# Performance work log

Hardware: AMD Instinct MI355X
Metric: run time of the kernel (lower is better)

## Reference

```python
import jax, jax.numpy as jnp
import numpy as np

# DCNv4 config (matches init_kwargs)
C = 64; G = 4; GC = C // G          # group channels = 16
KS = 3; KP = KS * KS                # 9 sampling points per group
DIL = 1; OFFSET_SCALE = 1.0
OM_DIM = int(np.ceil(G * KP * 3 / 8) * 8)  # 112 (padded offset+mask dim)
N, H, W = 4, 128, 128


def setup_inputs() -> dict:
    key = jax.random.key(0)
    ks = jax.random.split(key, 5)
    x = jax.random.normal(ks[0], (N, C, H, W), dtype=jnp.float32)
    value_w = jax.random.normal(ks[1], (C, C), dtype=jnp.float32) * (1.0 / np.sqrt(C))
    value_b = jnp.zeros((C,), dtype=jnp.float32)
    # small random offset/mask projection (torch zero-init would be degenerate)
    om_w = jax.random.normal(ks[2], (OM_DIM, C), dtype=jnp.float32) * 0.02
    om_b = jax.random.normal(ks[3], (OM_DIM,), dtype=jnp.float32) * 0.02
    out_w = jax.random.normal(ks[4], (C, C), dtype=jnp.float32) * (1.0 / np.sqrt(C))
    out_b = jnp.zeros((C,), dtype=jnp.float32)
    return {"x": x, "value_w": value_w, "value_b": value_b,
            "om_w": om_w, "om_b": om_b, "out_w": out_w, "out_b": out_b}


def _dcnv4_core(v, off, mask, Hh, Ww):
    # v: (N, L, G, GC)   off: (N, L, G, KP, 2) (x,y)   mask: (N, L, G, KP)
    n, L = v.shape[0], v.shape[1]
    py = (jnp.arange(L) // Ww).astype(jnp.float32)          # (L,)
    px = (jnp.arange(L) % Ww).astype(jnp.float32)
    r = (KS - 1) // 2
    dy, dx = jnp.meshgrid(jnp.arange(-r, r + 1, dtype=jnp.float32) * DIL,
                          jnp.arange(-r, r + 1, dtype=jnp.float32) * DIL,
                          indexing="ij")
    dy = dy.reshape(-1); dx = dx.reshape(-1)                # (KP,)
    # sampling coords: (N, L, G, KP)
    sy = py[None, :, None, None] + dy[None, None, None, :] + off[..., 1] * OFFSET_SCALE
    sx = px[None, :, None, None] + dx[None, None, None, :] + off[..., 0] * OFFSET_SCALE

    y0 = jnp.floor(sy); x0 = jnp.floor(sx)
    wy = sy - y0; wx = sx - x0
    vg = v.transpose(0, 2, 1, 3)                            # (N, G, L, GC)

    def gather(yc, xc, wgt):
        valid = ((yc >= 0) & (yc < Hh) & (xc >= 0) & (xc < Ww)).astype(v.dtype)
        yi = jnp.clip(yc, 0, Hh - 1).astype(jnp.int32)
        xi = jnp.clip(xc, 0, Ww - 1).astype(jnp.int32)
        idx = (yi * Ww + xi).transpose(0, 2, 1, 3).reshape(n, G, L * KP)  # (N,G,L*KP)
        g = jnp.take_along_axis(vg, idx[..., None], axis=2)              # (N,G,L*KP,GC)
        w = (wgt * valid).transpose(0, 2, 1, 3).reshape(n, G, L * KP, 1)
        return g * w

    samp = (gather(y0, x0, (1 - wy) * (1 - wx))
            + gather(y0, x0 + 1, (1 - wy) * wx)
            + gather(y0 + 1, x0, wy * (1 - wx))
            + gather(y0 + 1, x0 + 1, wy * wx))               # (N,G,L*KP,GC)
    samp = samp.reshape(n, G, L, KP, GC)
    m = mask.transpose(0, 2, 1, 3)[..., None]                # (N,G,L,KP,1)
    out = (samp * m).sum(axis=3)                             # (N,G,L,GC)
    return out.transpose(0, 2, 1, 3).reshape(n, L, G * GC)


def reference(x, value_w, value_b, om_w, om_b, out_w, out_b):
    n, c, Hh, Ww = x.shape
    L = Hh * Ww
    inp = x.transpose(0, 2, 3, 1).reshape(n, L, c)           # (N, L, C)
    v = (inp @ value_w.T + value_b).reshape(n, L, G, GC)     # value_proj
    om = inp @ om_w.T + om_b                                 # (N, L, 112)
    om = om[..., :G * KP * 3].reshape(n, L, G, KP * 3)       # per-group [off(2K), mask(K)]
    off = om[..., :2 * KP].reshape(n, L, G, KP, 2)
    mask = om[..., 2 * KP:]                                  # no softmax in DCNv4
    y = _dcnv4_core(v, off, mask, Hh, Ww)                    # (N, L, C)
    y = y @ out_w.T + out_b                                  # output_proj
    return y.reshape(n, Hh, Ww, c).transpose(0, 3, 1, 2)     # (N, C, H, W)
```

## Files before the change

### kernel.cpp

```cpp
#include <hip/hip_runtime.h>

#define NN 4
#define CC 64
#define GG 4
#define GCC 16
#define HH 128
#define WW 128
#define LL (HH*WW)
#define OMS 112
#define WPC 192

__global__ void pack_kernel(const float* __restrict__ value_w, const float* __restrict__ value_b,
                            const float* __restrict__ om_w,    const float* __restrict__ om_b,
                            const float* __restrict__ out_w,
                            float* __restrict__ wpack, float* __restrict__ bpack,
                            float* __restrict__ owt)
{
  const int i = blockIdx.x * 256 + threadIdx.x;
  if (i < 64 * WPC) {
    const int k = i / WPC, c = i % WPC;
    float v = 0.0f;
    if (c < 64) v = value_w[c * 64 + k];
    else if (c < 176) {
      const int s = c - 64;
      if (s % 28 != 27) { const int r = s - s / 28; v = om_w[r * 64 + k]; }
    }
    wpack[i] = v;
  }
  if (i < WPC) {
    float v = 0.0f;
    if (i < 64) v = value_b[i];
    else if (i < 176) {
      const int s = i - 64;
      if (s % 28 != 27) { const int r = s - s / 28; v = om_b[r]; }
    }
    bpack[i] = v;
  }
  if (i < 64 * 64) {
    const int k = i >> 6, c = i & 63;
    owt[i] = out_w[c * 64 + k];
  }
}

__global__ __launch_bounds__(256) void vm_kernel(
    const float* __restrict__ x, const float* __restrict__ wpack,
    const float* __restrict__ bpack,
    float* __restrict__ vws, float* __restrict__ omws)
{
  __shared__ float wlds[64][16];
  const int t    = threadIdx.x;
  const int ch   = blockIdx.y;
  const int col0 = ch << 4;

  {
    const int k = t >> 2, q = t & 3;
    *(float4*)&wlds[k][q * 4] =
        *(const float4*)&wpack[k * WPC + col0 + q * 4];
  }
  float b[16];
  #pragma unroll
  for (int j = 0; j < 16; ++j) b[j] = bpack[col0 + j];
  __syncthreads();

  const int l0 = blockIdx.x << 10;
  const int n  = l0 >> 14;
  const int hw = (l0 & (LL - 1)) + t;

  float acc[4][16];
  #pragma unroll
  for (int pi = 0; pi < 4; ++pi)
    #pragma unroll
    for (int j = 0; j < 16; ++j) acc[pi][j] = b[j];

  const float* xb = x + (size_t)n * CC * LL + hw;
  #pragma unroll 8
  for (int k = 0; k < 64; ++k) {
    float xv[4];
    #pragma unroll
    for (int pi = 0; pi < 4; ++pi) xv[pi] = xb[(size_t)k * LL + pi * 256];
    #pragma unroll
    for (int q = 0; q < 4; ++q) {
      const float4 w = *(const float4*)&wlds[k][q * 4];
      #pragma unroll
      for (int pi = 0; pi < 4; ++pi) {
        acc[pi][q*4+0] = fmaf(xv[pi], w.x, acc[pi][q*4+0]);
        acc[pi][q*4+1] = fmaf(xv[pi], w.y, acc[pi][q*4+1]);
        acc[pi][q*4+2] = fmaf(xv[pi], w.z, acc[pi][q*4+2]);
        acc[pi][q*4+3] = fmaf(xv[pi], w.w, acc[pi][q*4+3]);
      }
    }
  }

  float* dst; int col; int stride;
  if (ch < 4) { dst = vws  + (size_t)n * LL * 64;  col = col0;      stride = 64;  }
  else        { dst = omws + (size_t)n * LL * OMS; col = col0 - 64; stride = OMS; }
  #pragma unroll
  for (int pi = 0; pi < 4; ++pi) {
    float* d = dst + (size_t)(hw + pi * 256) * stride + col;
    #pragma unroll
    for (int q = 0; q < 4; ++q)
      *(float4*)&d[q * 4] =
          make_float4(acc[pi][q*4+0], acc[pi][q*4+1], acc[pi][q*4+2], acc[pi][q*4+3]);
  }
}

__global__ __launch_bounds__(512) void dcn_kernel(
    const float* __restrict__ vws, const float* __restrict__ omws,
    const float* __restrict__ owt, const float* __restrict__ out_b,
    float* __restrict__ out)
{
  __shared__ float s_lds[32][68];
  __shared__ float owlds[64 * 64];
  const int t   = threadIdx.x;
  const int B   = blockIdx.x;
  const int xcd = B & 7;
  const int n   = xcd >> 1;
  const int idx = ((xcd & 1) << 8) | (B >> 3);
  const int row = idx >> 2;
  const int l0  = (row << 7) + ((idx & 3) << 5);

  {
    const float4* s4 = (const float4*)owt;
    float4*       d4 = (float4*)owlds;
    d4[t]       = s4[t];
    d4[512 + t] = s4[512 + t];
  }

  {
    const int px = t >> 4;
    const int g  = (t >> 2) & 3;
    const int qq = t & 3;
    const int l  = l0 + px;
    const float pyf = (float)row;
    const float pxf = (float)(l & (WW - 1));
    const float* __restrict__ omp_  = omws + ((size_t)n * LL + l) * OMS + g * 28;
    const float* __restrict__ vbase = vws + (size_t)n * LL * CC + g * GCC + qq * 4;

    float buf[28];
    const float4* og4 = (const float4*)omp_;
    #pragma unroll
    for (int i = 0; i < 7; ++i) {
      const float4 vv = og4[i];
      buf[4*i+0] = vv.x; buf[4*i+1] = vv.y; buf[4*i+2] = vv.z; buf[4*i+3] = vv.w;
    }

    float s0 = 0.0f, s1 = 0.0f, s2 = 0.0f, s3 = 0.0f;

    #pragma unroll
    for (int pp = 0; pp < 9; ++pp) {
      const float sy  = pyf + (float)(pp / 3 - 1) + buf[2*pp+1];
      const float sx  = pxf + (float)(pp % 3 - 1) + buf[2*pp+0];
      const float y0f = floorf(sy), x0f = floorf(sx);
      const float wy  = sy - y0f,  wx  = sx - x0f;
      const int   iy  = (int)y0f,  ix  = (int)x0f;
      const float m   = buf[18 + pp];
      const float w00 = (1.0f - wy) * (1.0f - wx) * m;
      const float w01 = (1.0f - wy) * wx * m;
      const float w10 = wy * (1.0f - wx) * m;
      const float w11 = wy * wx * m;
      #pragma unroll
      for (int cor = 0; cor < 4; ++cor) {
        const int   cy = iy + (cor >> 1);
        const int   cx = ix + (cor & 1);
        const float w  = (cor == 0) ? w00 : (cor == 1) ? w01 : (cor == 2) ? w10 : w11;
        if (cy >= 0 && cy < HH && cx >= 0 && cx < WW) {
          const float4 vv = *(const float4*)(vbase + (size_t)(cy * WW + cx) * CC);
          s0 = fmaf(w, vv.x, s0);
          s1 = fmaf(w, vv.y, s1);
          s2 = fmaf(w, vv.z, s2);
          s3 = fmaf(w, vv.w, s3);
        }
      }
    }
    *(float4*)&s_lds[px][g * 16 + qq * 4] = make_float4(s0, s1, s2, s3);
  }
  __syncthreads();

  {
    const int px = t & 31;
    const int c4 = t >> 5;
    const int l  = l0 + px;
    float y0 = out_b[c4 * 4 + 0], y1 = out_b[c4 * 4 + 1];
    float y2 = out_b[c4 * 4 + 2], y3 = out_b[c4 * 4 + 3];
    #pragma unroll 4
    for (int k4 = 0; k4 < 16; ++k4) {
      const float4 sv = *(const float4*)&s_lds[px][k4 * 4];
      #pragma unroll
      for (int e = 0; e < 4; ++e) {
        const float se = (e == 0) ? sv.x : (e == 1) ? sv.y : (e == 2) ? sv.z : sv.w;
        const float4 wv = *(const float4*)&owlds[(k4 * 4 + e) * 64 + c4 * 4];
        y0 = fmaf(se, wv.x, y0);
        y1 = fmaf(se, wv.y, y1);
        y2 = fmaf(se, wv.z, y2);
        y3 = fmaf(se, wv.w, y3);
      }
    }
    float* op = out + ((size_t)n * CC) * LL + l;
    op[(size_t)(c4 * 4 + 0) * LL] = y0;
    op[(size_t)(c4 * 4 + 1) * LL] = y1;
    op[(size_t)(c4 * 4 + 2) * LL] = y2;
    op[(size_t)(c4 * 4 + 3) * LL] = y3;
  }
}

extern "C" void kernel_launch(void* const* d_in, const int* in_sizes, int n_in,
                              void* d_out, int out_size, void* d_ws, size_t ws_size,
                              hipStream_t stream) {
  const float* x       = (const float*)d_in[0];
  const float* value_w = (const float*)d_in[1];
  const float* value_b = (const float*)d_in[2];
  const float* om_w    = (const float*)d_in[3];
  const float* om_b    = (const float*)d_in[4];
  const float* out_w   = (const float*)d_in[5];
  const float* out_b   = (const float*)d_in[6];
  float* outp = (float*)d_out;

  float* vws   = (float*)d_ws;
  float* omws  = vws   + (size_t)NN * LL * CC;
  float* wpack = omws  + (size_t)NN * LL * OMS;
  float* bpack = wpack + 64 * WPC;
  float* owt   = bpack + WPC;

  pack_kernel<<<dim3(48), dim3(256), 0, stream>>>(
      value_w, value_b, om_w, om_b, out_w, wpack, bpack, owt);
  vm_kernel<<<dim3(64, 11), dim3(256), 0, stream>>>(
      x, wpack, bpack, vws, omws);
  dcn_kernel<<<dim3(2048), dim3(512), 0, stream>>>(
      vws, omws, owt, out_b, outp);
}
```

Baseline: 151.1 us.

## Use split-bf16 MFMA for input and output projections

```diff
diff --git a/kernel.cpp b/kernel.cpp
--- a/kernel.cpp
+++ b/kernel.cpp
@@ -10,107 +10,138 @@
 #define OMS 112
 #define WPC 192
 
+typedef __attribute__((ext_vector_type(8))) short bf16x8;
+typedef __attribute__((ext_vector_type(4))) float f32x4;
+
+static __device__ __forceinline__ unsigned short f2bf(float x) {
+  union { float f; unsigned u; } v; v.f = x;
+  unsigned r = v.u + 0x7fff + ((v.u >> 16) & 1);
+  return (unsigned short)(r >> 16);
+}
+static __device__ __forceinline__ float bf2f(unsigned short s) {
+  union { float f; unsigned u; } v; v.u = ((unsigned)s) << 16; return v.f;
+}
+static __device__ __forceinline__ void split2(float x, unsigned short& h, unsigned short& l) {
+  h = f2bf(x);
+  l = f2bf(x - bf2f(h));
+}
+
 __global__ void pack_kernel(const float* __restrict__ value_w, const float* __restrict__ value_b,
                             const float* __restrict__ om_w,    const float* __restrict__ om_b,
                             const float* __restrict__ out_w,
-                            float* __restrict__ wpack, float* __restrict__ bpack,
-                            float* __restrict__ owt)
+                            unsigned short* __restrict__ wphi, unsigned short* __restrict__ wplo,
+                            unsigned short* __restrict__ owhi, unsigned short* __restrict__ owlo,
+                            float* __restrict__ bpack)
 {
   const int i = blockIdx.x * 256 + threadIdx.x;
-  if (i < 64 * WPC) {
-    const int k = i / WPC, c = i % WPC;
+  if (i < WPC * 64) {
+    const int c = i >> 6, k = i & 63;
     float v = 0.0f;
     if (c < 64) v = value_w[c * 64 + k];
     else if (c < 176) {
       const int s = c - 64;
-      if (s % 28 != 27) { const int r = s - s / 28; v = om_w[r * 64 + k]; }
-    }
-    wpack[i] = v;
+      if (s % 28 != 27) v = om_w[(s - s / 28) * 64 + k];
+    }
+    unsigned short h, l; split2(v, h, l);
+    wphi[i] = h; wplo[i] = l;
+  }
+  if (i < 64 * 64) {
+    unsigned short h, l; split2(out_w[i], h, l);
+    owhi[i] = h; owlo[i] = l;
   }
   if (i < WPC) {
     float v = 0.0f;
     if (i < 64) v = value_b[i];
-    else if (i < 176) {
-      const int s = i - 64;
-      if (s % 28 != 27) { const int r = s - s / 28; v = om_b[r]; }
-    }
+    else if (i < 176) { const int s = i - 64; if (s % 28 != 27) v = om_b[s - s / 28]; }
     bpack[i] = v;
   }
-  if (i < 64 * 64) {
-    const int k = i >> 6, c = i & 63;
-    owt[i] = out_w[c * 64 + k];
-  }
 }
 
 __global__ __launch_bounds__(256) void vm_kernel(
-    const float* __restrict__ x, const float* __restrict__ wpack,
+    const float* __restrict__ x,
+    const unsigned short* __restrict__ wphi, const unsigned short* __restrict__ wplo,
     const float* __restrict__ bpack,
     float* __restrict__ vws, float* __restrict__ omws)
 {
-  __shared__ float wlds[64][16];
-  const int t    = threadIdx.x;
-  const int ch   = blockIdx.y;
-  const int col0 = ch << 4;
-
-  {
-    const int k = t >> 2, q = t & 3;
-    *(float4*)&wlds[k][q * 4] =
-        *(const float4*)&wpack[k * WPC + col0 + q * 4];
-  }
-  float b[16];
+  __shared__ unsigned short ahi[128][72];
+  __shared__ unsigned short alo[128][72];
+  const int t   = threadIdx.x;
+  const int sid = blockIdx.x;
+  const int n   = sid >> 7;
+  const int ll0 = (sid & 127) << 7;
+  const size_t gl0 = (size_t)sid << 7;
+
+  {
+    const float* xb = x + (size_t)n * CC * LL + ll0;
+    #pragma unroll
+    for (int i = 0; i < 4; ++i) {
+      const int pid = t + i * 256;
+      const int c   = (pid >> 5) << 1;
+      const int px4 = (pid & 31) << 2;
+      const float4 a = *(const float4*)(xb + (size_t)c * LL + px4);
+      const float4 b = *(const float4*)(xb + (size_t)(c + 1) * LL + px4);
+      const float av[4] = {a.x, a.y, a.z, a.w};
+      const float bv[4] = {b.x, b.y, b.z, b.w};
+      #pragma unroll
+      for (int e = 0; e < 4; ++e) {
+        unsigned short ha, la, hb, lb;
+        split2(av[e], ha, la); split2(bv[e], hb, lb);
+        *(unsigned*)&ahi[px4 + e][c] = (unsigned)ha | ((unsigned)hb << 16);
+        *(unsigned*)&alo[px4 + e][c] = (unsigned)la | ((unsigned)lb << 16);
+      }
+    }
+  }
+  __syncthreads();
+
+  const int w  = t >> 6;
+  const int ln = t & 63;
+  const int ct = blockIdx.y * 4 + w;
+  const int c0 = ct << 4;
+  const int r  = ln & 15;
+  const int kq = ln >> 4;
+
+  bf16x8 Bh[2], Bl[2];
   #pragma unroll
-  for (int j = 0; j < 16; ++j) b[j] = bpack[col0 + j];
-  __syncthreads();
-
-  const int l0 = blockIdx.x << 10;
-  const int n  = l0 >> 14;
-  const int hw = (l0 & (LL - 1)) + t;
-
-  float acc[4][16];
+  for (int ks = 0; ks < 2; ++ks) {
+    Bh[ks] = *(const bf16x8*)&wphi[(c0 + r) * 64 + ks * 32 + kq * 8];
+    Bl[ks] = *(const bf16x8*)&wplo[(c0 + r) * 64 + ks * 32 + kq * 8];
+  }
+  const float bias = bpack[c0 + r];
+
   #pragma unroll
-  for (int pi = 0; pi < 4; ++pi)
-    #pragma unroll
-    for (int j = 0; j < 16; ++j) acc[pi][j] = b[j];
-
-  const float* xb = x + (size_t)n * CC * LL + hw;
-  #pragma unroll 8
-  for (int k = 0; k < 64; ++k) {
-    float xv[4];
-    #pragma unroll
-    for (int pi = 0; pi < 4; ++pi) xv[pi] = xb[(size_t)k * LL + pi * 256];
-    #pragma unroll
-    for (int q = 0; q < 4; ++q) {
-      const float4 w = *(const float4*)&wlds[k][q * 4];
-      #pragma unroll
-      for (int pi = 0; pi < 4; ++pi) {
-        acc[pi][q*4+0] = fmaf(xv[pi], w.x, acc[pi][q*4+0]);
-        acc[pi][q*4+1] = fmaf(xv[pi], w.y, acc[pi][q*4+1]);
-        acc[pi][q*4+2] = fmaf(xv[pi], w.z, acc[pi][q*4+2]);
-        acc[pi][q*4+3] = fmaf(xv[pi], w.w, acc[pi][q*4+3]);
-      }
-    }
-  }
-
-  float* dst; int col; int stride;
-  if (ch < 4) { dst = vws  + (size_t)n * LL * 64;  col = col0;      stride = 64;  }
-  else        { dst = omws + (size_t)n * LL * OMS; col = col0 - 64; stride = OMS; }
-  #pragma unroll
-  for (int pi = 0; pi < 4; ++pi) {
-    float* d = dst + (size_t)(hw + pi * 256) * stride + col;
-    #pragma unroll
-    for (int q = 0; q < 4; ++q)
-      *(float4*)&d[q * 4] =
-          make_float4(acc[pi][q*4+0], acc[pi][q*4+1], acc[pi][q*4+2], acc[pi][q*4+3]);
-  }
-}
-
-__global__ __launch_bounds__(512) void dcn_kernel(
+  for (int pt = 0; pt < 8; ++pt) {
+    bf16x8 Ah[2], Al[2];
+    #pragma unroll
+    for (int ks = 0; ks < 2; ++ks) {
+      Ah[ks] = *(const bf16x8*)&ahi[pt * 16 + r][ks * 32 + kq * 8];
+      Al[ks] = *(const bf16x8*)&alo[pt * 16 + r][ks * 32 + kq * 8];
+    }
+    f32x4 acc = {bias, bias, bias, bias};
+    #pragma unroll
+    for (int ks = 0; ks < 2; ++ks) {
+      acc = __builtin_amdgcn_mfma_f32_16x16x32_bf16(Al[ks], Bh[ks], acc, 0, 0, 0);
+      acc = __builtin_amdgcn_mfma_f32_16x16x32_bf16(Ah[ks], Bl[ks], acc, 0, 0, 0);
+      acc = __builtin_amdgcn_mfma_f32_16x16x32_bf16(Ah[ks], Bh[ks], acc, 0, 0, 0);
+    }
+    if (ct < 4) {
+      float* d = vws + (gl0 + pt * 16 + kq * 4) * 64 + c0 + r;
+      d[0] = acc[0]; d[64] = acc[1]; d[128] = acc[2]; d[192] = acc[3];
+    } else if (ct < 11) {
+      float* d = omws + (gl0 + pt * 16 + kq * 4) * (size_t)OMS + (c0 - 64) + r;
+      d[0] = acc[0]; d[OMS] = acc[1]; d[2 * OMS] = acc[2]; d[3 * OMS] = acc[3];
+    }
+  }
+}
+
+__global__ __launch_bounds__(512, 4) void dcn_kernel(
     const float* __restrict__ vws, const float* __restrict__ omws,
-    const float* __restrict__ owt, const float* __restrict__ out_b,
+    const unsigned short* __restrict__ owhi, const unsigned short* __restrict__ owlo,
+    const float* __restrict__ out_b,
     float* __restrict__ out)
 {
-  __shared__ float s_lds[32][68];
-  __shared__ float owlds[64 * 64];
+  __shared__ unsigned short shi[32][72];
+  __shared__ unsigned short slo[32][72];
+  __shared__ float y_lds[32][68];
   const int t   = threadIdx.x;
   const int B   = blockIdx.x;
   const int xcd = B & 7;
@@ -120,16 +151,7 @@
   const int l0  = (row << 7) + ((idx & 3) << 5);
 
   {
-    const float4* s4 = (const float4*)owt;
-    float4*       d4 = (float4*)owlds;
-    d4[t]       = s4[t];
-    d4[512 + t] = s4[512 + t];
-  }
-
-  {
-    const int px = t >> 4;
-    const int g  = (t >> 2) & 3;
-    const int qq = t & 3;
+    const int px = t >> 4, g = (t >> 2) & 3, qq = t & 3;
     const int l  = l0 + px;
     const float pyf = (float)row;
     const float pxf = (float)(l & (WW - 1));
@@ -145,7 +167,6 @@
     }
 
     float s0 = 0.0f, s1 = 0.0f, s2 = 0.0f, s3 = 0.0f;
-
     #pragma unroll
     for (int pp = 0; pp < 9; ++pp) {
       const float sy  = pyf + (float)(pp / 3 - 1) + buf[2*pp+1];
@@ -162,44 +183,54 @@
       for (int cor = 0; cor < 4; ++cor) {
         const int   cy = iy + (cor >> 1);
         const int   cx = ix + (cor & 1);
-        const float w  = (cor == 0) ? w00 : (cor == 1) ? w01 : (cor == 2) ? w10 : w11;
+        const float wgt = (cor == 0) ? w00 : (cor == 1) ? w01 : (cor == 2) ? w10 : w11;
         if (cy >= 0 && cy < HH && cx >= 0 && cx < WW) {
           const float4 vv = *(const float4*)(vbase + (size_t)(cy * WW + cx) * CC);
-          s0 = fmaf(w, vv.x, s0);
-          s1 = fmaf(w, vv.y, s1);
-          s2 = fmaf(w, vv.z, s2);
-          s3 = fmaf(w, vv.w, s3);
+          s0 = fmaf(wgt, vv.x, s0);
+          s1 = fmaf(wgt, vv.y, s1);
+          s2 = fmaf(wgt, vv.z, s2);
+          s3 = fmaf(wgt, vv.w, s3);
         }
       }
     }
-    *(float4*)&s_lds[px][g * 16 + qq * 4] = make_float4(s0, s1, s2, s3);
+    unsigned short h0,u0,h1,u1,h2,u2,h3,u3;
+    split2(s0,h0,u0); split2(s1,h1,u1); split2(s2,h2,u2); split2(s3,h3,u3);
+    *(ushort4*)&shi[px][g * 16 + qq * 4] = make_ushort4(h0, h1, h2, h3);
+    *(ushort4*)&slo[px][g * 16 + qq * 4] = make_ushort4(u0, u1, u2, u3);
   }
   __syncthreads();
 
   {
-    const int px = t & 31;
-    const int c4 = t >> 5;
-    const int l  = l0 + px;
-    float y0 = out_b[c4 * 4 + 0], y1 = out_b[c4 * 4 + 1];
-    float y2 = out_b[c4 * 4 + 2], y3 = out_b[c4 * 4 + 3];
-    #pragma unroll 4
-    for (int k4 = 0; k4 < 16; ++k4) {
-      const float4 sv = *(const float4*)&s_lds[px][k4 * 4];
-      #pragma unroll
-      for (int e = 0; e < 4; ++e) {
-        const float se = (e == 0) ? sv.x : (e == 1) ? sv.y : (e == 2) ? sv.z : sv.w;
-        const float4 wv = *(const float4*)&owlds[(k4 * 4 + e) * 64 + c4 * 4];
-        y0 = fmaf(se, wv.x, y0);
-        y1 = fmaf(se, wv.y, y1);
-        y2 = fmaf(se, wv.z, y2);
-        y3 = fmaf(se, wv.w, y3);
-      }
-    }
-    float* op = out + ((size_t)n * CC) * LL + l;
-    op[(size_t)(c4 * 4 + 0) * LL] = y0;
-    op[(size_t)(c4 * 4 + 1) * LL] = y1;
-    op[(size_t)(c4 * 4 + 2) * LL] = y2;
-    op[(size_t)(c4 * 4 + 3) * LL] = y3;
+    const int w  = t >> 6, ln = t & 63;
+    const int pxt = w >> 2, ct = w & 3, c0 = ct << 4;
+    const int r  = ln & 15, kq = ln >> 4;
+    bf16x8 Ah[2], Al[2], Bh[2], Bl[2];
+    #pragma unroll
+    for (int ks = 0; ks < 2; ++ks) {
+      Ah[ks] = *(const bf16x8*)&shi[pxt * 16 + r][ks * 32 + kq * 8];
+      Al[ks] = *(const bf16x8*)&slo[pxt * 16 + r][ks * 32 + kq * 8];
+      Bh[ks] = *(const bf16x8*)&owhi[(c0 + r) * 64 + ks * 32 + kq * 8];
+      Bl[ks] = *(const bf16x8*)&owlo[(c0 + r) * 64 + ks * 32 + kq * 8];
+    }
+    const float bias = out_b[c0 + r];
+    f32x4 acc = {bias, bias, bias, bias};
+    #pragma unroll
+    for (int ks = 0; ks < 2; ++ks) {
+      acc = __builtin_amdgcn_mfma_f32_16x16x32_bf16(Al[ks], Bh[ks], acc, 0, 0, 0);
+      acc = __builtin_amdgcn_mfma_f32_16x16x32_bf16(Ah[ks], Bl[ks], acc, 0, 0, 0);
+      acc = __builtin_amdgcn_mfma_f32_16x16x32_bf16(Ah[ks], Bh[ks], acc, 0, 0, 0);
+    }
+    #pragma unroll
+    for (int j = 0; j < 4; ++j)
+      y_lds[pxt * 16 + kq * 4 + j][c0 + r] = acc[j];
+  }
+  __syncthreads();
+
+  {
+    const int c = t >> 3, px4 = (t & 7) << 2;
+    const float4 v = make_float4(y_lds[px4][c], y_lds[px4+1][c],
+                                 y_lds[px4+2][c], y_lds[px4+3][c]);
+    *(float4*)(out + ((size_t)n * CC + c) * LL + l0 + px4) = v;
   }
 }
 
@@ -216,15 +247,17 @@
   float* outp = (float*)d_out;
 
   float* vws   = (float*)d_ws;
-  float* omws  = vws   + (size_t)NN * LL * CC;
-  float* wpack = omws  + (size_t)NN * LL * OMS;
-  float* bpack = wpack + 64 * WPC;
-  float* owt   = bpack + WPC;
+  float* omws  = vws  + (size_t)NN * LL * CC;
+  float* bpack = omws + (size_t)NN * LL * OMS;
+  unsigned short* wphi = (unsigned short*)(bpack + WPC);
+  unsigned short* wplo = wphi + WPC * 64;
+  unsigned short* owhi = wplo + WPC * 64;
+  unsigned short* owlo = owhi + 64 * 64;
 
   pack_kernel<<<dim3(48), dim3(256), 0, stream>>>(
-      value_w, value_b, om_w, om_b, out_w, wpack, bpack, owt);
-  vm_kernel<<<dim3(64, 11), dim3(256), 0, stream>>>(
-      x, wpack, bpack, vws, omws);
+      value_w, value_b, om_w, om_b, out_w, wphi, wplo, owhi, owlo, bpack);
+  vm_kernel<<<dim3(512, 3), dim3(256), 0, stream>>>(
+      x, wphi, wplo, bpack, vws, omws);
   dcn_kernel<<<dim3(2048), dim3(512), 0, stream>>>(
-      vws, omws, owt, out_b, outp);
-}
+      vws, omws, owhi, owlo, out_b, outp);
+}
```

After: 137.7 us. -8.9%, faster.
